# Kernel optimization log

Measured on AMD Instinct MI355X. Metric: run time of the kernel, lower is better.

## Reference

```python
import jax, jax.numpy as jnp
import numpy as np

B, N, H = 64, 512, 768

def setup_inputs() -> dict:
    key = jax.random.key(0)
    k1, k2, k3 = jax.random.split(key, 3)
    arg_embeddings = jax.random.normal(k1, (B, N, H), dtype=jnp.float32)
    relation_W = jax.random.normal(k2, (H, H), dtype=jnp.float32) * 0.02
    relation_b = jax.random.normal(k3, (1,), dtype=jnp.float32) * 0.02
    return {"arg_embeddings": arg_embeddings, "relation_W": relation_W, "relation_b": relation_b}

def reference(arg_embeddings, relation_W, relation_b):
    # Bilinear pairwise scores: s[b,i,j] = x[b,i] @ W @ x[b,j] + bias
    xW = jnp.einsum('bih,hk->bik', arg_embeddings, relation_W)       # [B,N,H]
    scores = jnp.einsum('bik,bjk->bij', xW, arg_embeddings) + relation_b[0]
    # Original leaves diagonal entries at 0 (loop skips i == j)
    n = scores.shape[1]
    eye = jnp.eye(n, dtype=bool)
    scores = jnp.where(eye[None, :, :], 0.0, scores)
    relation_weights = jax.nn.softmax(scores, axis=-1)               # [B,N,N]
    relation_features = jnp.einsum('bij,bjh->bih', relation_weights, arg_embeddings)
    return relation_features
```

## Files before the change

kernel.cpp:

```cpp
#include <hip/hip_runtime.h>
#include <hip/hip_bf16.h>
#include <math.h>

static constexpr int B_ = 64;
static constexpr int N_ = 512;
static constexpr int H_ = 768;

typedef float f32x16 __attribute__((ext_vector_type(16)));
typedef short bf16x8 __attribute__((ext_vector_type(8)));

static __device__ __forceinline__ f32x16 mfma32(bf16x8 a, bf16x8 b, f32x16 c) {
    return __builtin_amdgcn_mfma_f32_32x32x16_bf16(a, b, c, 0, 0, 0);
}

static __device__ __forceinline__ uint32_t pack_hi2(float f0, float f1) {
    uint32_t u0 = __float_as_uint(f0), u1 = __float_as_uint(f1);
    return (u1 & 0xFFFF0000u) | (u0 >> 16);
}
static __device__ __forceinline__ uint32_t pack_lo2(float f0, float f1) {
    uint32_t u0 = __float_as_uint(f0), u1 = __float_as_uint(f1);
    float l0 = f0 - __uint_as_float(u0 & 0xFFFF0000u);
    float l1 = f1 - __uint_as_float(u1 & 0xFFFF0000u);
    uint32_t v0 = __float_as_uint(l0), v1 = __float_as_uint(l1);
    return (v1 & 0xFFFF0000u) | (v0 >> 16);
}

#define R32(reg, half) (((reg) & 3) + 8 * ((reg) >> 2) + 4 * (half))

__global__ __launch_bounds__(256, 2) void gemm_xw_mfma(const float* __restrict__ X,
                                                       const float* __restrict__ W,
                                                       uint32_t* __restrict__ C) {
    __shared__ __align__(16) unsigned short Ahi[128][40];
    __shared__ __align__(16) unsigned short Alo[128][40];
    __shared__ __align__(16) unsigned short Bhi[128][40];
    __shared__ __align__(16) unsigned short Blo[128][40];

    const int t    = threadIdx.x;
    const int w    = t >> 6;
    const int lane = t & 63;
    const int half = lane >> 5;
    const int ln   = lane & 31;
    const int wi   = w & 1;
    const int wh   = w >> 1;

    const int l   = blockIdx.x;
    const int xcd = l & 7;
    const int r   = l >> 3;
    const int nx  = r % 6;
    const int yq  = r / 6;
    const int m0  = (xcd + 8 * yq) * 128;
    const int n0  = nx * 128;

    const int ar  = t >> 3;
    const int ac4 = t & 7;
    const int bj  = t & 127;
    const int bkb = (t >> 7) * 16;

    f32x16 acc[2][2];
    f32x16 zf = {};
    #pragma unroll
    for (int is = 0; is < 2; ++is)
        #pragma unroll
        for (int hs = 0; hs < 2; ++hs) acc[is][hs] = zf;

    for (int k0 = 0; k0 < H_; k0 += 32) {
        float4 av[4];
        #pragma unroll
        for (int u = 0; u < 4; ++u)
            av[u] = *(const float4*)&X[(size_t)(m0 + ar + u * 32) * H_ + k0 + ac4 * 4];
        const float* wp = W + (size_t)(k0 + bkb) * H_ + n0 + bj;
        float wv[16];
        #pragma unroll
        for (int kk = 0; kk < 16; ++kk)
            wv[kk] = wp[(size_t)kk * H_];

        uint2 ahp[4], alp[4];
        #pragma unroll
        for (int u = 0; u < 4; ++u) {
            ahp[u] = make_uint2(pack_hi2(av[u].x, av[u].y), pack_hi2(av[u].z, av[u].w));
            alp[u] = make_uint2(pack_lo2(av[u].x, av[u].y), pack_lo2(av[u].z, av[u].w));
        }
        uint4 bhp[2], blp[2];
        #pragma unroll
        for (int q = 0; q < 2; ++q) {
            const int b8 = q * 8;
            bhp[q] = make_uint4(pack_hi2(wv[b8 + 0], wv[b8 + 1]), pack_hi2(wv[b8 + 2], wv[b8 + 3]),
                                pack_hi2(wv[b8 + 4], wv[b8 + 5]), pack_hi2(wv[b8 + 6], wv[b8 + 7]));
            blp[q] = make_uint4(pack_lo2(wv[b8 + 0], wv[b8 + 1]), pack_lo2(wv[b8 + 2], wv[b8 + 3]),
                                pack_lo2(wv[b8 + 4], wv[b8 + 5]), pack_lo2(wv[b8 + 6], wv[b8 + 7]));
        }

        __syncthreads();
        #pragma unroll
        for (int u = 0; u < 4; ++u) {
            *(uint2*)&Ahi[ar + u * 32][ac4 * 4] = ahp[u];
            *(uint2*)&Alo[ar + u * 32][ac4 * 4] = alp[u];
        }
        #pragma unroll
        for (int q = 0; q < 2; ++q) {
            *(uint4*)&Bhi[bj][bkb + q * 8] = bhp[q];
            *(uint4*)&Blo[bj][bkb + q * 8] = blp[q];
        }
        __syncthreads();

        #pragma unroll
        for (int ks = 0; ks < 2; ++ks) {
            const int koff = ks * 16 + half * 8;
            bf16x8 ah[2], al[2], bh[2], bl[2];
            #pragma unroll
            for (int is = 0; is < 2; ++is) {
                ah[is] = *(const bf16x8*)&Ahi[wi * 64 + is * 32 + ln][koff];
                al[is] = *(const bf16x8*)&Alo[wi * 64 + is * 32 + ln][koff];
            }
            #pragma unroll
            for (int hs = 0; hs < 2; ++hs) {
                bh[hs] = *(const bf16x8*)&Bhi[wh * 64 + hs * 32 + ln][koff];
                bl[hs] = *(const bf16x8*)&Blo[wh * 64 + hs * 32 + ln][koff];
            }
            #pragma unroll
            for (int is = 0; is < 2; ++is)
                #pragma unroll
                for (int hs = 0; hs < 2; ++hs) {
                    acc[is][hs] = mfma32(ah[is], bh[hs], acc[is][hs]);
                    acc[is][hs] = mfma32(ah[is], bl[hs], acc[is][hs]);
                    acc[is][hs] = mfma32(al[is], bh[hs], acc[is][hs]);
                }
        }
    }

    #pragma unroll
    for (int is = 0; is < 2; ++is)
        #pragma unroll
        for (int hs = 0; hs < 2; ++hs)
            #pragma unroll
            for (int reg = 0; reg < 16; ++reg) {
                float v  = acc[is][hs][reg];
                float v1 = __shfl_xor(v, 1);
                if ((ln & 1) == 0) {
                    const int gi = m0 + wi * 64 + is * 32 + R32(reg, half);
                    const int gj = n0 + wh * 64 + hs * 32 + ln;
                    uint32_t* orow = C + (size_t)gi * H_;
                    const int g = gj >> 3;
                    const int p = (gj >> 1) & 3;
                    orow[g * 8 + p]     = pack_hi2(v, v1);
                    orow[g * 8 + 4 + p] = pack_lo2(v, v1);
                }
            }
}

__global__ __launch_bounds__(256, 2) void attn_scores(const float* __restrict__ X,
                                                      const uint32_t* __restrict__ Q32,
                                                      const float* __restrict__ bias_p,
                                                      __hip_bfloat16* __restrict__ P) {
    __shared__ __align__(16) unsigned short Khi[128][72];
    __shared__ __align__(16) unsigned short Klo[128][72];
    __shared__ __align__(16) unsigned short Qs[64][136];
    __shared__ float smax[4][64];
    __shared__ float ssum[4][64];
    __shared__ float sscale[4][64];

    const int t    = threadIdx.x;
    const int w    = t >> 6;
    const int lane = t & 63;
    const int half = lane >> 5;
    const int ln   = lane & 31;

    const int l  = blockIdx.x;
    const int q  = l >> 3;
    const int b  = (l & 7) + 8 * (q >> 3);
    const int I0 = (q & 7) * 64;
    const float bias = bias_p[0];

    const float* xb = X + (size_t)b * N_ * H_;
    const uint32_t* qbase = Q32 + ((size_t)b * N_ + I0) * H_;

    const int krb = t >> 4;
    const int kc4 = t & 15;

    f32x16 acc[2][4];
    f32x16 zf = {};
    #pragma unroll
    for (int is = 0; is < 2; ++is)
        #pragma unroll
        for (int jb = 0; jb < 4; ++jb) acc[is][jb] = zf;

    float4 kv[8];
    #pragma unroll
    for (int u = 0; u < 8; ++u)
        kv[u] = *(const float4*)&xb[(size_t)(krb + 16 * u) * H_ + kc4 * 4];

    for (int kph = 0; kph < 12; ++kph) {
        #pragma unroll
        for (int jb = 0; jb < 4; ++jb) {
            uint2 hp[8], lp[8];
            #pragma unroll
            for (int u = 0; u < 8; ++u) {
                hp[u] = make_uint2(pack_hi2(kv[u].x, kv[u].y), pack_hi2(kv[u].z, kv[u].w));
                lp[u] = make_uint2(pack_lo2(kv[u].x, kv[u].y), pack_lo2(kv[u].z, kv[u].w));
            }
            __syncthreads();
            #pragma unroll
            for (int u = 0; u < 8; ++u) {
                *(uint2*)&Khi[krb + 16 * u][kc4 * 4] = hp[u];
                *(uint2*)&Klo[krb + 16 * u][kc4 * 4] = lp[u];
            }
            if (jb == 0) {
                uint32_t* qlds = (uint32_t*)&Qs[0][0];
                #pragma unroll
                for (int u = 0; u < 4; ++u) {
                    const int r   = (t >> 4) + 16 * u;
                    const int w16 = t & 15;
                    uint4 v = *(const uint4*)&qbase[(size_t)r * H_ + kph * 64 + w16 * 4];
                    *(uint4*)&qlds[r * 68 + w16 * 4] = v;
                }
            }
            __syncthreads();

            {
                const int np = kph * 4 + jb + 1;
                if (np < 48) {
                    const int nk = np >> 2, nj = np & 3;
                    #pragma unroll
                    for (int u = 0; u < 8; ++u)
                        kv[u] = *(const float4*)&xb[(size_t)(nj * 128 + krb + 16 * u) * H_ +
                                                    nk * 64 + kc4 * 4];
                }
            }

            #pragma unroll
            for (int ks = 0; ks < 4; ++ks) {
                const int gq = ks * 2 + half;
                bf16x8 qh[2], ql[2];
                #pragma unroll
                for (int is = 0; is < 2; ++is) {
                    qh[is] = *(const bf16x8*)&Qs[is * 32 + ln][gq * 16];
                    ql[is] = *(const bf16x8*)&Qs[is * 32 + ln][gq * 16 + 8];
                }
                const int koff = ks * 16 + half * 8;
                bf16x8 kh = *(const bf16x8*)&Khi[w * 32 + ln][koff];
                bf16x8 kl = *(const bf16x8*)&Klo[w * 32 + ln][koff];
                #pragma unroll
                for (int is = 0; is < 2; ++is) {
                    acc[is][jb] = mfma32(qh[is], kh, acc[is][jb]);
                    acc[is][jb] = mfma32(qh[is], kl, acc[is][jb]);
                    acc[is][jb] = mfma32(ql[is], kh, acc[is][jb]);
                }
            }
        }
    }

    const int gj = w * 32 + ln;
    #pragma unroll
    for (int is = 0; is < 2; ++is)
        #pragma unroll
        for (int jb = 0; jb < 4; ++jb)
            #pragma unroll
            for (int reg = 0; reg < 16; ++reg) {
                float v = acc[is][jb][reg] + bias;
                int gi = I0 + is * 32 + R32(reg, half);
                if (gi == jb * 128 + gj) v = 0.0f;
                acc[is][jb][reg] = v;
            }

    float mrow[2][16];
    #pragma unroll
    for (int is = 0; is < 2; ++is)
        #pragma unroll
        for (int reg = 0; reg < 16; ++reg) {
            float m = acc[is][0][reg];
            #pragma unroll
            for (int jb = 1; jb < 4; ++jb) m = fmaxf(m, acc[is][jb][reg]);
            #pragma unroll
            for (int d = 1; d < 32; d <<= 1) m = fmaxf(m, __shfl_xor(m, d));
            mrow[is][reg] = m;
            if (ln == 0) smax[w][is * 32 + R32(reg, half)] = m;
        }

    #pragma unroll
    for (int is = 0; is < 2; ++is)
        #pragma unroll
        for (int reg = 0; reg < 16; ++reg) {
            float s = 0.f;
            #pragma unroll
            for (int jb = 0; jb < 4; ++jb) {
                float e = __expf(acc[is][jb][reg] - mrow[is][reg]);
                acc[is][jb][reg] = e;
                s += e;
            }
            #pragma unroll
            for (int d = 1; d < 32; d <<= 1) s += __shfl_xor(s, d);
            if (ln == 0) ssum[w][is * 32 + R32(reg, half)] = s;
        }
    __syncthreads();

    if (t < 64) {
        float M = smax[0][t];
        #pragma unroll
        for (int w2 = 1; w2 < 4; ++w2) M = fmaxf(M, smax[w2][t]);
        float L = 0.f;
        #pragma unroll
        for (int w2 = 0; w2 < 4; ++w2) L += ssum[w2][t] * __expf(smax[w2][t] - M);
        float invL = 1.0f / L;
        #pragma unroll
        for (int w2 = 0; w2 < 4; ++w2) sscale[w2][t] = __expf(smax[w2][t] - M) * invL;
    }
    __syncthreads();

    __hip_bfloat16* Pb = P + (size_t)b * N_ * N_;
    #pragma unroll
    for (int is = 0; is < 2; ++is)
        #pragma unroll
        for (int reg = 0; reg < 16; ++reg) {
            int row = is * 32 + R32(reg, half);
            float sc = sscale[w][row];
            #pragma unroll
            for (int jb = 0; jb < 4; ++jb) {
                float p = acc[is][jb][reg] * sc;
                Pb[(size_t)(I0 + row) * N_ + jb * 128 + w * 32 + ln] = __float2bfloat16(p);
            }
        }
}

__global__ __launch_bounds__(256, 2) void pv_gemm(const float* __restrict__ X,
                                                  const __hip_bfloat16* __restrict__ P,
                                                  float* __restrict__ O) {
    __shared__ __align__(16) unsigned short Pt[128][40];
    __shared__ __align__(16) unsigned short Vt[256][40];

    const int t    = threadIdx.x;
    const int w    = t >> 6;
    const int lane = t & 63;
    const int half = lane >> 5;
    const int ln   = lane & 31;
    const int wi   = w & 1;
    const int wh   = w >> 1;

    const int l     = blockIdx.x;
    const int r     = l >> 3;
    const int inner = r % 12;
    const int b     = (l & 7) + 8 * (r / 12);
    const int H0    = (inner % 3) * 256;
    const int I0    = (inner / 3) * 128;

    const unsigned short* Pb = (const unsigned short*)P + (size_t)b * N_ * N_;
    const float* xb = X + (size_t)b * N_ * H_;

    f32x16 acc[2][4];
    f32x16 zf = {};
    #pragma unroll
    for (int is = 0; is < 2; ++is)
        #pragma unroll
        for (int hs = 0; hs < 4; ++hs) acc[is][hs] = zf;

    for (int j0 = 0; j0 < N_; j0 += 32) {
        __syncthreads();
        #pragma unroll
        for (int u = 0; u < 2; ++u) {
            int idx = t + 256 * u;
            int rr  = idx >> 2;
            int c8  = idx & 3;
            uint4 v = *(const uint4*)&Pb[(size_t)(I0 + rr) * N_ + j0 + c8 * 8];
            *(uint4*)&Pt[rr][c8 * 8] = v;
        }
        {
            const float* xc = xb + (size_t)j0 * H_ + H0 + t;
            #pragma unroll
            for (int jj = 0; jj < 32; jj += 2) {
                float f0 = xc[(size_t)jj * H_];
                float f1 = xc[(size_t)(jj + 1) * H_];
                __hip_bfloat16 b0 = __float2bfloat16(f0);
                __hip_bfloat16 b1 = __float2bfloat16(f1);
                unsigned short u0, u1;
                __builtin_memcpy(&u0, &b0, 2);
                __builtin_memcpy(&u1, &b1, 2);
                *(uint32_t*)&Vt[t][jj] = ((uint32_t)u1 << 16) | u0;
            }
        }
        __syncthreads();
        #pragma unroll
        for (int ks = 0; ks < 2; ++ks) {
            const int koff = ks * 16 + half * 8;
            bf16x8 a[2], v[4];
            #pragma unroll
            for (int is = 0; is < 2; ++is)
                a[is] = *(const bf16x8*)&Pt[wi * 64 + is * 32 + ln][koff];
            #pragma unroll
            for (int hs = 0; hs < 4; ++hs)
                v[hs] = *(const bf16x8*)&Vt[wh * 128 + hs * 32 + ln][koff];
            #pragma unroll
            for (int is = 0; is < 2; ++is)
                #pragma unroll
                for (int hs = 0; hs < 4; ++hs)
                    acc[is][hs] = mfma32(a[is], v[hs], acc[is][hs]);
        }
    }

    float* Ob = O + (size_t)b * N_ * H_;
    #pragma unroll
    for (int is = 0; is < 2; ++is)
        #pragma unroll
        for (int hs = 0; hs < 4; ++hs)
            #pragma unroll
            for (int reg = 0; reg < 16; ++reg) {
                int row = I0 + wi * 64 + is * 32 + R32(reg, half);
                int col = H0 + wh * 128 + hs * 32 + ln;
                Ob[(size_t)row * H_ + col] = acc[is][hs][reg];
            }
}

extern "C" void kernel_launch(void* const* d_in, const int* in_sizes, int n_in,
                              void* d_out, int out_size, void* d_ws, size_t ws_size,
                              hipStream_t stream) {
    const float* x    = (const float*)d_in[0];
    const float* W    = (const float*)d_in[1];
    const float* bias = (const float*)d_in[2];

    gemm_xw_mfma<<<dim3(1536), 256, 0, stream>>>(x, W, (uint32_t*)d_out);
    attn_scores<<<dim3(512), 256, 0, stream>>>(
        x, (const uint32_t*)d_out, bias, (__hip_bfloat16*)d_ws);
    pv_gemm<<<dim3(768), 256, 0, stream>>>(
        x, (const __hip_bfloat16*)d_ws, (float*)d_out);
}
```

Before: 431.4 us.

## Enlarge XW GEMM M-tile and software-pipeline PV GEMM with 64-wide K steps

The XW GEMM block tile grows from 128 to 256 rows, with wider 8-float A loads, and the launch halves to 768 blocks, so each W tile is reused across more rows. The PV GEMM now steps K by 64 per iteration and prefetches the next P and X tiles into registers before the MFMA loop, overlapping global loads with compute and halving the number of barriers. The cost is much higher register pressure (a 32-float prefetch buffer and twice as many accumulators), which may reduce occupancy or cause spills, plus larger LDS tiles.

```diff
diff --git a/kernel.cpp b/kernel.cpp
--- a/kernel.cpp
+++ b/kernel.cpp
@@ -25,13 +25,22 @@
     return (v1 & 0xFFFF0000u) | (v0 >> 16);
 }
 
+static __device__ __forceinline__ uint32_t bf16pair(float f0, float f1) {
+    __hip_bfloat16 b0 = __float2bfloat16(f0);
+    __hip_bfloat16 b1 = __float2bfloat16(f1);
+    unsigned short u0, u1;
+    __builtin_memcpy(&u0, &b0, 2);
+    __builtin_memcpy(&u1, &b1, 2);
+    return ((uint32_t)u1 << 16) | u0;
+}
+
 #define R32(reg, half) (((reg) & 3) + 8 * ((reg) >> 2) + 4 * (half))
 
 __global__ __launch_bounds__(256, 2) void gemm_xw_mfma(const float* __restrict__ X,
                                                        const float* __restrict__ W,
                                                        uint32_t* __restrict__ C) {
-    __shared__ __align__(16) unsigned short Ahi[128][40];
-    __shared__ __align__(16) unsigned short Alo[128][40];
+    __shared__ __align__(16) unsigned short Ahi[256][40];
+    __shared__ __align__(16) unsigned short Alo[256][40];
     __shared__ __align__(16) unsigned short Bhi[128][40];
     __shared__ __align__(16) unsigned short Blo[128][40];
 
@@ -48,37 +57,42 @@
     const int r   = l >> 3;
     const int nx  = r % 6;
     const int yq  = r / 6;
-    const int m0  = (xcd + 8 * yq) * 128;
+    const int m0  = (xcd + 8 * yq) * 256;
     const int n0  = nx * 128;
 
-    const int ar  = t >> 3;
-    const int ac4 = t & 7;
+    const int rw = t >> 2;
+    const int k8 = (t & 3) * 8;
     const int bj  = t & 127;
     const int bkb = (t >> 7) * 16;
 
-    f32x16 acc[2][2];
+    f32x16 acc[4][2];
     f32x16 zf = {};
     #pragma unroll
-    for (int is = 0; is < 2; ++is)
+    for (int is = 0; is < 4; ++is)
         #pragma unroll
         for (int hs = 0; hs < 2; ++hs) acc[is][hs] = zf;
 
     for (int k0 = 0; k0 < H_; k0 += 32) {
-        float4 av[4];
-        #pragma unroll
-        for (int u = 0; u < 4; ++u)
-            av[u] = *(const float4*)&X[(size_t)(m0 + ar + u * 32) * H_ + k0 + ac4 * 4];
+        float4 a0[4], a1[4];
+        #pragma unroll
+        for (int u = 0; u < 4; ++u) {
+            const float* ap = &X[(size_t)(m0 + rw + 64 * u) * H_ + k0 + k8];
+            a0[u] = *(const float4*)ap;
+            a1[u] = *(const float4*)(ap + 4);
+        }
         const float* wp = W + (size_t)(k0 + bkb) * H_ + n0 + bj;
         float wv[16];
         #pragma unroll
         for (int kk = 0; kk < 16; ++kk)
             wv[kk] = wp[(size_t)kk * H_];
 
-        uint2 ahp[4], alp[4];
+        uint4 ahp[4], alp[4];
         #pragma unroll
         for (int u = 0; u < 4; ++u) {
-            ahp[u] = make_uint2(pack_hi2(av[u].x, av[u].y), pack_hi2(av[u].z, av[u].w));
-            alp[u] = make_uint2(pack_lo2(av[u].x, av[u].y), pack_lo2(av[u].z, av[u].w));
+            ahp[u] = make_uint4(pack_hi2(a0[u].x, a0[u].y), pack_hi2(a0[u].z, a0[u].w),
+                                pack_hi2(a1[u].x, a1[u].y), pack_hi2(a1[u].z, a1[u].w));
+            alp[u] = make_uint4(pack_lo2(a0[u].x, a0[u].y), pack_lo2(a0[u].z, a0[u].w),
+                                pack_lo2(a1[u].x, a1[u].y), pack_lo2(a1[u].z, a1[u].w));
         }
         uint4 bhp[2], blp[2];
         #pragma unroll
@@ -93,8 +107,8 @@
         __syncthreads();
         #pragma unroll
         for (int u = 0; u < 4; ++u) {
-            *(uint2*)&Ahi[ar + u * 32][ac4 * 4] = ahp[u];
-            *(uint2*)&Alo[ar + u * 32][ac4 * 4] = alp[u];
+            *(uint4*)&Ahi[rw + 64 * u][k8] = ahp[u];
+            *(uint4*)&Alo[rw + 64 * u][k8] = alp[u];
         }
         #pragma unroll
         for (int q = 0; q < 2; ++q) {
@@ -106,11 +120,11 @@
         #pragma unroll
         for (int ks = 0; ks < 2; ++ks) {
             const int koff = ks * 16 + half * 8;
-            bf16x8 ah[2], al[2], bh[2], bl[2];
-            #pragma unroll
-            for (int is = 0; is < 2; ++is) {
-                ah[is] = *(const bf16x8*)&Ahi[wi * 64 + is * 32 + ln][koff];
-                al[is] = *(const bf16x8*)&Alo[wi * 64 + is * 32 + ln][koff];
+            bf16x8 ah[4], al[4], bh[2], bl[2];
+            #pragma unroll
+            for (int is = 0; is < 4; ++is) {
+                ah[is] = *(const bf16x8*)&Ahi[wi * 128 + is * 32 + ln][koff];
+                al[is] = *(const bf16x8*)&Alo[wi * 128 + is * 32 + ln][koff];
             }
             #pragma unroll
             for (int hs = 0; hs < 2; ++hs) {
@@ -118,7 +132,7 @@
                 bl[hs] = *(const bf16x8*)&Blo[wh * 64 + hs * 32 + ln][koff];
             }
             #pragma unroll
-            for (int is = 0; is < 2; ++is)
+            for (int is = 0; is < 4; ++is)
                 #pragma unroll
                 for (int hs = 0; hs < 2; ++hs) {
                     acc[is][hs] = mfma32(ah[is], bh[hs], acc[is][hs]);
@@ -129,7 +143,7 @@
     }
 
     #pragma unroll
-    for (int is = 0; is < 2; ++is)
+    for (int is = 0; is < 4; ++is)
         #pragma unroll
         for (int hs = 0; hs < 2; ++hs)
             #pragma unroll
@@ -137,7 +151,7 @@
                 float v  = acc[is][hs][reg];
                 float v1 = __shfl_xor(v, 1);
                 if ((ln & 1) == 0) {
-                    const int gi = m0 + wi * 64 + is * 32 + R32(reg, half);
+                    const int gi = m0 + wi * 128 + is * 32 + R32(reg, half);
                     const int gj = n0 + wh * 64 + hs * 32 + ln;
                     uint32_t* orow = C + (size_t)gi * H_;
                     const int g = gj >> 3;
@@ -208,10 +222,10 @@
                 uint32_t* qlds = (uint32_t*)&Qs[0][0];
                 #pragma unroll
                 for (int u = 0; u < 4; ++u) {
-                    const int r   = (t >> 4) + 16 * u;
+                    const int rr  = (t >> 4) + 16 * u;
                     const int w16 = t & 15;
-                    uint4 v = *(const uint4*)&qbase[(size_t)r * H_ + kph * 64 + w16 * 4];
-                    *(uint4*)&qlds[r * 68 + w16 * 4] = v;
+                    uint4 v = *(const uint4*)&qbase[(size_t)rr * H_ + kph * 64 + w16 * 4];
+                    *(uint4*)&qlds[rr * 68 + w16 * 4] = v;
                 }
             }
             __syncthreads();
@@ -324,8 +338,8 @@
 __global__ __launch_bounds__(256, 2) void pv_gemm(const float* __restrict__ X,
                                                   const __hip_bfloat16* __restrict__ P,
                                                   float* __restrict__ O) {
-    __shared__ __align__(16) unsigned short Pt[128][40];
-    __shared__ __align__(16) unsigned short Vt[256][40];
+    __shared__ __align__(16) unsigned short Pt[128][72];
+    __shared__ __align__(16) unsigned short Vt[256][72];
 
     const int t    = threadIdx.x;
     const int w    = t >> 6;
@@ -343,7 +357,11 @@
     const int I0    = (inner / 3) * 128;
 
     const unsigned short* Pb = (const unsigned short*)P + (size_t)b * N_ * N_;
-    const float* xb = X + (size_t)b * N_ * H_;
+    const float* xb   = X + (size_t)b * N_ * H_;
+    const float* xcol = xb + H0 + t;
+
+    const int pr = t >> 3;
+    const int pc = t & 7;
 
     f32x16 acc[2][4];
     f32x16 zf = {};
@@ -352,33 +370,56 @@
         #pragma unroll
         for (int hs = 0; hs < 4; ++hs) acc[is][hs] = zf;
 
-    for (int j0 = 0; j0 < N_; j0 += 32) {
+    uint4 pPre[4];
+    float vPre[32];
+    #pragma unroll
+    for (int u = 0; u < 4; ++u)
+        pPre[u] = *(const uint4*)&Pb[(size_t)(I0 + pr + 32 * u) * N_ + pc * 8];
+    #pragma unroll
+    for (int jj = 0; jj < 32; ++jj)
+        vPre[jj] = xcol[(size_t)jj * H_];
+
+    for (int j0 = 0; j0 < N_; j0 += 64) {
+        float vCur[32];
+        #pragma unroll
+        for (int jj = 0; jj < 32; ++jj)
+            vCur[jj] = xcol[(size_t)(j0 + 32 + jj) * H_];
+
+        uint32_t vp[16];
+        #pragma unroll
+        for (int m = 0; m < 16; ++m)
+            vp[m] = bf16pair(vPre[2 * m], vPre[2 * m + 1]);
+
         __syncthreads();
         #pragma unroll
-        for (int u = 0; u < 2; ++u) {
-            int idx = t + 256 * u;
-            int rr  = idx >> 2;
-            int c8  = idx & 3;
-            uint4 v = *(const uint4*)&Pb[(size_t)(I0 + rr) * N_ + j0 + c8 * 8];
-            *(uint4*)&Pt[rr][c8 * 8] = v;
-        }
-        {
-            const float* xc = xb + (size_t)j0 * H_ + H0 + t;
-            #pragma unroll
-            for (int jj = 0; jj < 32; jj += 2) {
-                float f0 = xc[(size_t)jj * H_];
-                float f1 = xc[(size_t)(jj + 1) * H_];
-                __hip_bfloat16 b0 = __float2bfloat16(f0);
-                __hip_bfloat16 b1 = __float2bfloat16(f1);
-                unsigned short u0, u1;
-                __builtin_memcpy(&u0, &b0, 2);
-                __builtin_memcpy(&u1, &b1, 2);
-                *(uint32_t*)&Vt[t][jj] = ((uint32_t)u1 << 16) | u0;
-            }
-        }
+        for (int u = 0; u < 4; ++u)
+            *(uint4*)&Pt[pr + 32 * u][pc * 8] = pPre[u];
+        #pragma unroll
+        for (int qq = 0; qq < 4; ++qq)
+            *(uint4*)&Vt[t][qq * 8] =
+                make_uint4(vp[4 * qq], vp[4 * qq + 1], vp[4 * qq + 2], vp[4 * qq + 3]);
+        uint32_t vq[16];
+        #pragma unroll
+        for (int m = 0; m < 16; ++m)
+            vq[m] = bf16pair(vCur[2 * m], vCur[2 * m + 1]);
+        #pragma unroll
+        for (int qq = 0; qq < 4; ++qq)
+            *(uint4*)&Vt[t][32 + qq * 8] =
+                make_uint4(vq[4 * qq], vq[4 * qq + 1], vq[4 * qq + 2], vq[4 * qq + 3]);
         __syncthreads();
-        #pragma unroll
-        for (int ks = 0; ks < 2; ++ks) {
+
+        if (j0 + 64 < N_) {
+            #pragma unroll
+            for (int u = 0; u < 4; ++u)
+                pPre[u] = *(const uint4*)&Pb[(size_t)(I0 + pr + 32 * u) * N_ +
+                                             (j0 + 64) + pc * 8];
+            #pragma unroll
+            for (int jj = 0; jj < 32; ++jj)
+                vPre[jj] = xcol[(size_t)(j0 + 64 + jj) * H_];
+        }
+
+        #pragma unroll
+        for (int ks = 0; ks < 4; ++ks) {
             const int koff = ks * 16 + half * 8;
             bf16x8 a[2], v[4];
             #pragma unroll
@@ -415,7 +456,7 @@
     const float* W    = (const float*)d_in[1];
     const float* bias = (const float*)d_in[2];
 
-    gemm_xw_mfma<<<dim3(1536), 256, 0, stream>>>(x, W, (uint32_t*)d_out);
+    gemm_xw_mfma<<<dim3(768), 256, 0, stream>>>(x, W, (uint32_t*)d_out);
     attn_scores<<<dim3(512), 256, 0, stream>>>(
         x, (const uint32_t*)d_out, bias, (__hip_bfloat16*)d_ws);
     pv_gemm<<<dim3(768), 256, 0, stream>>>(
```

New measurement: 459.3 us. 6.5% more time.
